# Kernel tuning notes

Hardware: AMD Instinct MI355X
Metric: run time of the kernel (lower is better)

Reference implementation:

```python
import jax, jax.numpy as jnp
import numpy as np


def setup_inputs() -> dict:
    key = jax.random.key(0)
    k1, k2, k3 = jax.random.split(key, 3)
    B, C, H, W = 32, 192, 64, 64
    L = 64  # number of unique quantization levels in the sos codebook
    x = jax.random.normal(k1, (B, C, H, W), dtype=jnp.float32) * 4.0
    means = jax.random.normal(k2, (B, C, H, W), dtype=jnp.float32)
    # sorted 1-D codebook of unique quantizer levels (sos.unique_values)
    codebook = jnp.sort(jax.random.normal(k3, (L,), dtype=jnp.float32) * 4.0)
    return {"x": x, "means": means, "codebook": codebook}


def _nearest_level(r, codebook):
    """Vectorized version of transform_map: for each element of r, the index of
    the nearest codebook value (argmin |codebook - r|), using searchsorted on
    the sorted codebook instead of a dense [N, L] distance matrix."""
    L = codebook.shape[0]
    pos = jnp.clip(jnp.searchsorted(codebook, r), 1, L - 1)  # right neighbor
    left = codebook[pos - 1]
    right = codebook[pos]
    return jnp.where(r - left <= right - r, pos - 1, pos)  # int32 symbols


def reference(x, means, codebook):
    # quantize(mode='symbols'): subtract means, map each value to the index of
    # the nearest codebook level (the map_sos_cdf dict lookup / argmin loop).
    r = x - means
    symbols = _nearest_level(r, codebook)          # [B,C,H,W] int32
    # dequantize: map symbols back to float levels (map_cdf_sos) and add means.
    y_hat = jnp.take(codebook, symbols) + means    # [B,C,H,W] float32
    return symbols, y_hat
```

## Files before the change

### kernel.cpp

```cpp
#include <hip/hip_runtime.h>


typedef float v4f __attribute__((ext_vector_type(4)));

struct Tree {
    float c31;
    float c15, c47;
    float c07, c23, c39, c55;
    float c03, c11, c19, c27, c35, c43, c51, c59;
};

__device__ __forceinline__ void nearest(const Tree& t, float cbreg,
                                        float r, float m,
                                        float& sym, float& y)
{
    int p = (t.c31 < r) ? 32 : 0;

    float v = (p & 32) ? t.c47 : t.c15;
    p += (v < r) ? 16 : 0;

    float u0 = (p & 16) ? t.c23 : t.c07;
    float u1 = (p & 16) ? t.c55 : t.c39;
    v = (p & 32) ? u1 : u0;
    p += (v < r) ? 8 : 0;

    float w0 = (p & 8) ? t.c11 : t.c03;
    float w1 = (p & 8) ? t.c27 : t.c19;
    float w2 = (p & 8) ? t.c43 : t.c35;
    float w3 = (p & 8) ? t.c59 : t.c51;
    float w4 = (p & 16) ? w1 : w0;
    float w5 = (p & 16) ? w3 : w2;
    v = (p & 32) ? w5 : w4;
    p += (v < r) ? 4 : 0;

    v = __shfl(cbreg, p + 1);
    p += (v < r) ? 2 : 0;
    v = __shfl(cbreg, p);
    p += (v < r) ? 1 : 0;

    p = min(max(p, 1), 63);
    const float left  = __shfl(cbreg, p - 1);
    const float right = __shfl(cbreg, p);
    const bool tie = (r - left) <= (right - r);
    sym = (float)(tie ? p - 1 : p);
    y   = (tie ? left : right) + m;
}

__global__ __launch_bounds__(256, 4) void quant_dequant_kernel(
    const v4f* __restrict__ x4,
    const v4f* __restrict__ m4,
    const float* __restrict__ codebook,
    v4f* __restrict__ sym_out,
    v4f* __restrict__ yhat_out,
    int n8)
{
    const float cbreg = codebook[threadIdx.x & 63];

    Tree t;
    t.c31 = codebook[31];
    t.c15 = codebook[15]; t.c47 = codebook[47];
    t.c07 = codebook[7];  t.c23 = codebook[23];
    t.c39 = codebook[39]; t.c55 = codebook[55];
    t.c03 = codebook[3];  t.c11 = codebook[11];
    t.c19 = codebook[19]; t.c27 = codebook[27];
    t.c35 = codebook[35]; t.c43 = codebook[43];
    t.c51 = codebook[51]; t.c59 = codebook[59];

    const int i = blockIdx.x * blockDim.x + threadIdx.x;
    if (i >= n8) return;
    const int j = i + n8;

    const v4f xa = x4[i];
    const v4f ma = m4[i];
    const v4f xb = x4[j];
    const v4f mb = m4[j];

    v4f sa, ya, sb, yb;
#pragma unroll
    for (int k = 0; k < 4; ++k) {
        float s0, y0, s1, y1;
        nearest(t, cbreg, xa[k] - ma[k], ma[k], s0, y0);
        nearest(t, cbreg, xb[k] - mb[k], mb[k], s1, y1);
        sa[k] = s0; ya[k] = y0;
        sb[k] = s1; yb[k] = y1;
    }

    __builtin_nontemporal_store(sa, &sym_out[i]);
    __builtin_nontemporal_store(ya, &yhat_out[i]);
    __builtin_nontemporal_store(sb, &sym_out[j]);
    __builtin_nontemporal_store(yb, &yhat_out[j]);
}

extern "C" void kernel_launch(void* const* d_in, const int* in_sizes, int n_in,
                              void* d_out, int out_size, void* d_ws, size_t ws_size,
                              hipStream_t stream)
{
    const float* x     = (const float*)d_in[0];
    const float* means = (const float*)d_in[1];
    const float* cb    = (const float*)d_in[2];

    const int n  = in_sizes[0];
    const int n8 = n / 8;

    float* out = (float*)d_out;

    const int block = 256;
    const int grid  = (n8 + block - 1) / block;

    quant_dequant_kernel<<<grid, block, 0, stream>>>(
        (const v4f*)x, (const v4f*)means, cb,
        (v4f*)out, (v4f*)(out + n), n8);
}
```

Before: 345.4 us.

## Replace shuffle-based final search levels with LDS vector codebook lookup

```diff
diff --git a/kernel.cpp b/kernel.cpp
--- a/kernel.cpp
+++ b/kernel.cpp
@@ -10,9 +10,7 @@
     float c03, c11, c19, c27, c35, c43, c51, c59;
 };
 
-__device__ __forceinline__ void nearest(const Tree& t, float cbreg,
-                                        float r, float m,
-                                        float& sym, float& y)
+__device__ __forceinline__ int tree4(const Tree& t, float r)
 {
     int p = (t.c31 < r) ? 32 : 0;
 
@@ -32,18 +30,7 @@
     float w5 = (p & 16) ? w3 : w2;
     v = (p & 32) ? w5 : w4;
     p += (v < r) ? 4 : 0;
-
-    v = __shfl(cbreg, p + 1);
-    p += (v < r) ? 2 : 0;
-    v = __shfl(cbreg, p);
-    p += (v < r) ? 1 : 0;
-
-    p = min(max(p, 1), 63);
-    const float left  = __shfl(cbreg, p - 1);
-    const float right = __shfl(cbreg, p);
-    const bool tie = (r - left) <= (right - r);
-    sym = (float)(tie ? p - 1 : p);
-    y   = (tie ? left : right) + m;
+    return p;
 }
 
 __global__ __launch_bounds__(256, 4) void quant_dequant_kernel(
@@ -52,9 +39,11 @@
     const float* __restrict__ codebook,
     v4f* __restrict__ sym_out,
     v4f* __restrict__ yhat_out,
-    int n8)
+    int n4)
 {
-    const float cbreg = codebook[threadIdx.x & 63];
+    __shared__ __align__(16) float s_cb[64];
+    const int tid = threadIdx.x;
+    if (tid < 64) s_cb[tid] = codebook[tid];
 
     Tree t;
     t.c31 = codebook[31];
@@ -66,29 +55,62 @@
     t.c35 = codebook[35]; t.c43 = codebook[43];
     t.c51 = codebook[51]; t.c59 = codebook[59];
 
-    const int i = blockIdx.x * blockDim.x + threadIdx.x;
-    if (i >= n8) return;
-    const int j = i + n8;
+    __syncthreads();
+
+    const int i = (blockIdx.x * 256 + tid) * 2;
+    if (i >= n4) return;
 
     const v4f xa = x4[i];
     const v4f ma = m4[i];
-    const v4f xb = x4[j];
-    const v4f mb = m4[j];
+    const v4f xb = x4[i + 1];
+    const v4f mb = m4[i + 1];
 
-    v4f sa, ya, sb, yb;
+    float r[8], mm[8];
 #pragma unroll
     for (int k = 0; k < 4; ++k) {
-        float s0, y0, s1, y1;
-        nearest(t, cbreg, xa[k] - ma[k], ma[k], s0, y0);
-        nearest(t, cbreg, xb[k] - mb[k], mb[k], s1, y1);
-        sa[k] = s0; ya[k] = y0;
-        sb[k] = s1; yb[k] = y1;
+        r[k]     = xa[k] - ma[k];  mm[k]     = ma[k];
+        r[4 + k] = xb[k] - mb[k];  mm[4 + k] = mb[k];
     }
 
+    int p4[8];
+#pragma unroll
+    for (int e = 0; e < 8; ++e) p4[e] = tree4(t, r[e]);
+
+    v4f  q[8];
+    float vm1[8];
+#pragma unroll
+    for (int e = 0; e < 8; ++e) {
+        q[e]   = *(const v4f*)&s_cb[p4[e]];
+        vm1[e] = s_cb[max(p4[e] - 1, 0)];
+    }
+
+    float sym[8], yv[8];
+#pragma unroll
+    for (int e = 0; e < 8; ++e) {
+        const v4f qq = q[e];
+        const float rr = r[e];
+        const int lb = p4[e] + ((qq[0] < rr) ? 1 : 0) + ((qq[1] < rr) ? 1 : 0)
+                             + ((qq[2] < rr) ? 1 : 0) + ((qq[3] < rr) ? 1 : 0);
+        const int pos = min(max(lb, 1), 63);
+        const int tt  = pos - p4[e];
+        const float left  = (tt == 1) ? qq[0] : (tt == 2) ? qq[1]
+                          : (tt == 3) ? qq[2] : vm1[e];
+        const float right = (tt == 1) ? qq[1] : (tt == 2) ? qq[2]
+                          : (tt == 3) ? qq[3] : qq[0];
+        const bool tie = (rr - left) <= (right - rr);
+        sym[e] = (float)(tie ? pos - 1 : pos);
+        yv[e]  = (tie ? left : right) + mm[e];
+    }
+
+    const v4f sa = { sym[0], sym[1], sym[2], sym[3] };
+    const v4f sb = { sym[4], sym[5], sym[6], sym[7] };
+    const v4f ya = { yv[0],  yv[1],  yv[2],  yv[3]  };
+    const v4f yb = { yv[4],  yv[5],  yv[6],  yv[7]  };
+
     __builtin_nontemporal_store(sa, &sym_out[i]);
+    __builtin_nontemporal_store(sb, &sym_out[i + 1]);
     __builtin_nontemporal_store(ya, &yhat_out[i]);
-    __builtin_nontemporal_store(sb, &sym_out[j]);
-    __builtin_nontemporal_store(yb, &yhat_out[j]);
+    __builtin_nontemporal_store(yb, &yhat_out[i + 1]);
 }
 
 extern "C" void kernel_launch(void* const* d_in, const int* in_sizes, int n_in,
@@ -100,14 +122,15 @@
     const float* cb    = (const float*)d_in[2];
 
     const int n  = in_sizes[0];
-    const int n8 = n / 8;
+    const int n4 = n / 4;
 
     float* out = (float*)d_out;
 
     const int block = 256;
-    const int grid  = (n8 + block - 1) / block;
+    const int f4_per_block = block * 2;
+    const int grid = (n4 + f4_per_block - 1) / f4_per_block;
 
     quant_dequant_kernel<<<grid, block, 0, stream>>>(
         (const v4f*)x, (const v4f*)means, cb,
-        (v4f*)out, (v4f*)(out + n), n8);
+        (v4f*)out, (v4f*)(out + n), n4);
 }
```

Measured after the change: 360.0 us. 1.04x slower.
